# Kernel optimization log

Hardware: AMD Instinct MI355X
Metric: run time of the kernel (lower is better)

Reference implementation:

```python
import jax, jax.numpy as jnp
import numpy as np

K = 9          # kernel_size (number of KNN neighbours), dilation=1
SCALAR = 20.0  # scalar in _build_explain
EPS = 1e-10


def setup_inputs() -> dict:
    key = jax.random.key(0)
    ks = jax.random.split(key, 9)
    B, C, H, W = 16, 192, 28, 28
    Cout, r = 384, 16
    f = lambda k, s, sc: jax.random.normal(k, s, jnp.float32) * sc
    return {
        "x": f(ks[0], (B, C, H, W), 1.0),
        "w_edge": f(ks[1], (Cout, 2 * C), 0.05),  # 1x1 conv on concat[x_i, x_j-x_i]
        "b_edge": f(ks[2], (Cout,), 0.05),
        "w1": f(ks[3], (C // r, C), 0.1),          # CBAM channel MLP (shared)
        "b1": f(ks[4], (C // r,), 0.1),
        "w2": f(ks[5], (C, C // r), 0.1),
        "b2": f(ks[6], (C,), 0.1),
        "w_sp": f(ks[7], (1, 2, 7, 7), 0.1),       # CBAM spatial 7x7 conv
        "b_sp": f(ks[8], (1,), 0.1),
    }


def _cbam(x, w1, b1, w2, b2, w_sp, b_sp):
    # Standard CBAM: channel gate (avg+max pooled -> shared MLP -> sigmoid)
    # then spatial gate (channel mean/max -> 7x7 conv -> sigmoid).
    mlp = lambda v: jax.nn.relu(v @ w1.T + b1) @ w2.T + b2
    ch = jax.nn.sigmoid(mlp(x.mean((2, 3))) + mlp(x.max((2, 3))))
    x = x * ch[:, :, None, None]
    sp_in = jnp.stack([x.mean(1), x.max(1)], axis=1)  # (B,2,H,W)
    sp = jax.lax.conv_general_dilated(sp_in, w_sp, (1, 1), [(3, 3), (3, 3)])
    return x * jax.nn.sigmoid(sp + b_sp[None, :, None, None])


def _build_explain(att_x):
    B, C, H, W = att_x.shape
    a = jax.nn.softmax(att_x.reshape(B, C, H * W), axis=2)
    a = a / (a.max(axis=2, keepdims=True) + EPS)
    return (2.0 * a - 1.0) / (2.0 * SCALAR) + 1.0  # (B,C,N)


def _knn_idx(xf):
    # DenseDilatedKnnGraph: L2-normalize over channels, pairwise sq-dist, topk.
    xn = xf / jnp.maximum(jnp.linalg.norm(xf, axis=1, keepdims=True), 1e-12)
    xt = jnp.swapaxes(xn, 1, 2)                      # (B,N,C)
    sq = jnp.sum(xt * xt, axis=-1)                   # (B,N)
    dist = sq[:, :, None] - 2.0 * jnp.einsum("bnc,bmc->bnm", xt, xt) + sq[:, None, :]
    _, idx = jax.lax.top_k(-dist, K)                 # nn_idx = edge_index[0], (B,N,K)
    return idx


def reference(x, w_edge, b_edge, w1, b1, w2, b2, w_sp, b_sp):
    B, C, H, W = x.shape
    N = H * W
    xf = x.reshape(B, C, N)
    idx = _knn_idx(xf)                               # dynamic KNN graph (B,N,K)
    att = _build_explain(_cbam(x, w1, b1, w2, b2, w_sp, b_sp))
    xf = xf * att
    # EdgeConv2d: x_i = center (edge_index[1] is arange -> broadcast),
    # x_j gathered by neighbour indices.
    x_i = xf[:, :, :, None]                           # (B,C,N,1)
    x_e = jnp.broadcast_to(x_i, (B, C, N, K))
    i_e = jnp.broadcast_to(idx[:, None, :, :], (B, C, N, K))
    x_j = jnp.take_along_axis(x_e, i_e, axis=2)       # (B,C,N,K)
    feat = jnp.concatenate([x_e, x_j - x_i], axis=1)  # (B,2C,N,K)
    out = jnp.einsum("oc,bcnk->bonk", w_edge, feat) + b_edge[None, :, None, None]
    out = jax.nn.relu(out)                            # BasicConv: 1x1 conv + relu
    out = out.max(axis=-1)                            # max over neighbours (B,O,N)
    return out.reshape(B, -1, H, W)
```

## Files before the change

kernel.cpp:

```cpp
#include <hip/hip_runtime.h>
#include <math.h>

#define HW 784
#define Cc 192
#define Bb 16
#define CO 384
#define KK 9
#define OG 8

typedef __attribute__((ext_vector_type(8))) short bf16x8;
typedef __attribute__((ext_vector_type(4))) float f32x4;

__device__ __forceinline__ unsigned f2ord(float f){
  unsigned u = __float_as_uint(f);
  return (u & 0x80000000u) ? ~u : (u | 0x80000000u);
}

__device__ __forceinline__ unsigned short b16rne(float v){
  unsigned u = __float_as_uint(v);
  unsigned r = u + 0x7FFFu + ((u >> 16) & 1u);
  return (unsigned short)(r >> 16);
}

__global__ void k_chstats(const float* __restrict__ x, float* __restrict__ chm, float* __restrict__ chx){
  int wid = threadIdx.x >> 6, lane = threadIdx.x & 63;
  int r = blockIdx.x * 4 + wid;
  const float* row = x + (size_t)r * HW;
  float s = 0.f, m = -3.4e38f;
  for (int n = lane; n < HW; n += 64){ float v = row[n]; s += v; m = fmaxf(m, v); }
  for (int off = 32; off; off >>= 1){ s += __shfl_xor(s, off); m = fmaxf(m, __shfl_xor(m, off)); }
  if (lane == 0){ chm[r] = s / (float)HW; chx[r] = m; }
}

__global__ void k_mlp(const float* __restrict__ chm, const float* __restrict__ chx,
                      const float* __restrict__ w1, const float* __restrict__ b1,
                      const float* __restrict__ w2, const float* __restrict__ b2,
                      float* __restrict__ chv){
  int b = blockIdx.x, t = threadIdx.x;
  __shared__ float vm[Cc], vx[Cc], hp[2][12];
  if (t < Cc){ vm[t] = chm[b*Cc + t]; vx[t] = chx[b*Cc + t]; }
  __syncthreads();
  if (t < 24){
    int h = t % 12;
    const float* src = (t < 12) ? vm : vx;
    float a = b1[h];
    for (int c = 0; c < Cc; ++c) a += src[c] * w1[h*Cc + c];
    hp[t/12][h] = fmaxf(a, 0.f);
  }
  __syncthreads();
  if (t < Cc){
    float a = 2.f * b2[t];
    for (int h = 0; h < 12; ++h) a += (hp[0][h] + hp[1][h]) * w2[t*12 + h];
    chv[b*Cc + t] = 1.f / (1.f + expf(-a));
  }
}

__global__ void k_spin(const float* __restrict__ x, const float* __restrict__ chv,
                       float* __restrict__ amean, float* __restrict__ amax){
  int b = blockIdx.x >> 2;
  int n = ((blockIdx.x & 3) << 8) + threadIdx.x;
  if (n >= HW) return;
  const float* xb = x + (size_t)b*Cc*HW + n;
  const float* cb = chv + b*Cc;
  float s = 0.f, m = -3.4e38f;
  for (int c = 0; c < Cc; ++c){ float v = xb[(size_t)c*HW] * cb[c]; s += v; m = fmaxf(m, v); }
  amean[b*HW + n] = s / (float)Cc;
  amax[b*HW + n]  = m;
}

__global__ void k_conv(const float* __restrict__ amean, const float* __restrict__ amax,
                       const float* __restrict__ wsp, const float* __restrict__ bsp,
                       float* __restrict__ satt){
  int b = blockIdx.x >> 2;
  int n = ((blockIdx.x & 3) << 8) + threadIdx.x;
  if (n >= HW) return;
  int yy = n / 28, xx = n % 28;
  float a = 0.f;
  for (int ky = 0; ky < 7; ++ky){
    int iy = yy + ky - 3; if (iy < 0 || iy >= 28) continue;
    for (int kx = 0; kx < 7; ++kx){
      int ix = xx + kx - 3; if (ix < 0 || ix >= 28) continue;
      int ii = b*HW + iy*28 + ix;
      a += amean[ii]*wsp[ky*7 + kx] + amax[ii]*wsp[49 + ky*7 + kx];
    }
  }
  satt[b*HW + n] = 1.f / (1.f + expf(-(a + bsp[0])));
}

__global__ __launch_bounds__(256) void k_att(const float* __restrict__ x, const float* __restrict__ chv,
                                             const float* __restrict__ satt, float* __restrict__ xatt){
  int bc = blockIdx.x;
  int b = bc / Cc;
  int t = threadIdx.x, wid = t >> 6, lane = t & 63;
  const float* xr = x + (size_t)bc * HW;
  const float* sr = satt + b * HW;
  float ch = chv[bc];
  float xv[4], vv[4];
  float lmax = -3.4e38f;
  #pragma unroll
  for (int j = 0; j < 4; ++j){
    int n = t + 256*j;
    if (n < HW){
      xv[j] = xr[n];
      float t1 = xv[j] * ch;
      vv[j] = t1 * sr[n];
      lmax = fmaxf(lmax, vv[j]);
    }
  }
  __shared__ float red[8];
  for (int off = 32; off; off >>= 1) lmax = fmaxf(lmax, __shfl_xor(lmax, off));
  if (!lane) red[wid] = lmax;
  __syncthreads();
  float vmax = fmaxf(fmaxf(red[0], red[1]), fmaxf(red[2], red[3]));
  float ls = 0.f;
  #pragma unroll
  for (int j = 0; j < 4; ++j){
    int n = t + 256*j;
    if (n < HW){ vv[j] = expf(vv[j] - vmax); ls += vv[j]; }
  }
  for (int off = 32; off; off >>= 1) ls += __shfl_xor(ls, off);
  if (!lane) red[4 + wid] = ls;
  __syncthreads();
  float S = red[4] + red[5] + red[6] + red[7];
  float inv = 1.f / (1.f + 1e-10f * S);
  #pragma unroll
  for (int j = 0; j < 4; ++j){
    int n = t + 256*j;
    if (n < HW){
      float a = vv[j] * inv;
      xatt[(size_t)bc*HW + n] = xv[j] * ((2.f*a - 1.f)*0.025f + 1.f);
    }
  }
}

__global__ void k_norm(const float* __restrict__ x, float* __restrict__ nrm){
  int b = blockIdx.x >> 2;
  int n = ((blockIdx.x & 3) << 8) + threadIdx.x;
  if (n >= HW) return;
  const float* xb = x + (size_t)b*Cc*HW + n;
  float s = 0.f;
  for (int c = 0; c < Cc; ++c){ float v = xb[(size_t)c*HW]; s += v*v; }
  nrm[b*HW + n] = fmaxf(sqrtf(s), 1e-12f);
}

__global__ __launch_bounds__(256) void k_cvt(const float* __restrict__ x, const float* __restrict__ nrm,
                                             unsigned short* __restrict__ Xth, unsigned short* __restrict__ Xtl){
  int b = blockIdx.z, c0 = blockIdx.y*64, n0 = blockIdx.x*64;
  __shared__ float T[64][65];
  int t = threadIdx.x;
  int nl = (t & 15) * 4, cl = t >> 4;
  const float* xb = x + (size_t)b*Cc*HW;
  #pragma unroll
  for (int r = 0; r < 4; ++r){
    int c_loc = cl + r*16;
    int n = n0 + nl;
    float4 v = (n < HW) ? *(const float4*)(xb + (size_t)(c0 + c_loc)*HW + n) : make_float4(0,0,0,0);
    *(float4*)&T[c_loc][nl] = v;
  }
  __syncthreads();
  int nr = t >> 2, q = t & 3;
  int n_g = n0 + nr;
  if (n_g >= HW) return;
  float nv = nrm ? nrm[b*HW + n_g] : 1.f;
  unsigned int hw_[8], lw_[8];
  #pragma unroll
  for (int j = 0; j < 8; ++j){
    float v0 = T[q*16 + 2*j][nr] / nv;
    float v1 = T[q*16 + 2*j + 1][nr] / nv;
    unsigned short h0 = b16rne(v0), h1 = b16rne(v1);
    float l0 = v0 - __uint_as_float((unsigned)h0 << 16);
    float l1 = v1 - __uint_as_float((unsigned)h1 << 16);
    hw_[j] = (unsigned)h0 | ((unsigned)h1 << 16);
    lw_[j] = (unsigned)b16rne(l0) | ((unsigned)b16rne(l1) << 16);
  }
  size_t base = ((size_t)b*HW + n_g)*Cc + c0 + q*16;
  *(uint4*)(Xth + base)     = make_uint4(hw_[0], hw_[1], hw_[2], hw_[3]);
  *(uint4*)(Xth + base + 8) = make_uint4(hw_[4], hw_[5], hw_[6], hw_[7]);
  *(uint4*)(Xtl + base)     = make_uint4(lw_[0], lw_[1], lw_[2], lw_[3]);
  *(uint4*)(Xtl + base + 8) = make_uint4(lw_[4], lw_[5], lw_[6], lw_[7]);
}

__global__ __launch_bounds__(256) void k_gram(const unsigned short* __restrict__ Xth,
                                              const unsigned short* __restrict__ Xtl,
                                              float* __restrict__ D){
  int b = blockIdx.z;
  int n0 = blockIdx.y*128, m0 = blockIdx.x*128;
  __shared__ unsigned short Als[8192];
  __shared__ unsigned short Bls[8192];
  int t = threadIdx.x, w = t >> 6, l = t & 63;
  int wr = w >> 1, wc = w & 1;
  f32x4 acc[4][4] = {};
  int nn = t >> 1, half = t & 1;
  size_t bb = (size_t)b*HW*Cc;
  int ra = n0 + nn; if (ra > HW-1) ra = HW-1;
  int rb = m0 + nn; if (rb > HW-1) rb = HW-1;

  for (int cc = 0; cc < 9; ++cc){
    int seg = cc/3, kc0 = (cc%3)*64;
    const unsigned short* As_ = (seg < 2 ? Xth : Xtl) + bb;
    const unsigned short* Bs_ = (seg == 1 ? Xtl : Xth) + bb;
    const uint4* ga = (const uint4*)(As_ + (size_t)ra*Cc + kc0 + half*32);
    const uint4* gb = (const uint4*)(Bs_ + (size_t)rb*Cc + kc0 + half*32);
    uint4 va0 = ga[0], va1 = ga[1], va2 = ga[2], va3 = ga[3];
    uint4 vb0 = gb[0], vb1 = gb[1], vb2 = gb[2], vb3 = gb[3];
    __syncthreads();
    int base = nn*128 + half*64;
    int sw = (nn & 7) << 4;
    *(uint4*)((char*)Als + ((base      ) ^ sw)) = va0;
    *(uint4*)((char*)Als + ((base + 16 ) ^ sw)) = va1;
    *(uint4*)((char*)Als + ((base + 32 ) ^ sw)) = va2;
    *(uint4*)((char*)Als + ((base + 48 ) ^ sw)) = va3;
    *(uint4*)((char*)Bls + ((base      ) ^ sw)) = vb0;
    *(uint4*)((char*)Bls + ((base + 16 ) ^ sw)) = vb1;
    *(uint4*)((char*)Bls + ((base + 32 ) ^ sw)) = vb2;
    *(uint4*)((char*)Bls + ((base + 48 ) ^ sw)) = vb3;
    __syncthreads();
    #pragma unroll
    for (int ks = 0; ks < 2; ++ks){
      bf16x8 af[4], bfr[4];
      int kb = ks*64 + (l >> 4)*16;
      #pragma unroll
      for (int mt = 0; mt < 4; ++mt){
        int rl = wr*64 + mt*16 + (l & 15);
        int off = (rl*128 + kb) ^ ((rl & 7) << 4);
        af[mt] = *(const bf16x8*)((const char*)Als + off);
      }
      #pragma unroll
      for (int nt = 0; nt < 4; ++nt){
        int cl2 = wc*64 + nt*16 + (l & 15);
        int off = (cl2*128 + kb) ^ ((cl2 & 7) << 4);
        bfr[nt] = *(const bf16x8*)((const char*)Bls + off);
      }
      #pragma unroll
      for (int mt = 0; mt < 4; ++mt)
        #pragma unroll
        for (int nt = 0; nt < 4; ++nt)
          acc[mt][nt] = __builtin_amdgcn_mfma_f32_16x16x32_bf16(af[mt], bfr[nt], acc[mt][nt], 0, 0, 0);
    }
  }
  #pragma unroll
  for (int mt = 0; mt < 4; ++mt){
    #pragma unroll
    for (int nt = 0; nt < 4; ++nt){
      int col = m0 + wc*64 + nt*16 + (l & 15);
      if (col >= HW) continue;
      int row0 = n0 + wr*64 + mt*16 + ((l >> 4) << 2);
      #pragma unroll
      for (int r = 0; r < 4; ++r){
        int row = row0 + r;
        if (row < HW) D[((size_t)b*HW + row)*HW + col] = -acc[mt][nt][r];
      }
    }
  }
}

__global__ __launch_bounds__(256) void k_select(const float* __restrict__ D, int* __restrict__ idxo){
  int wid = threadIdx.x >> 6, lane = threadIdx.x & 63;
  int row = blockIdx.x * 4 + wid;
  const float* Dr = D + (size_t)row * HW;
  float dvv[13]; int mvv[13];
  #pragma unroll
  for (int i = 0; i < 13; ++i){
    int m = lane + 64*i;
    dvv[i] = (m < HW) ? Dr[m] : 3.4e38f;
    mvv[i] = m;
  }
  for (int k = 0; k < KK; ++k){
    float bd = dvv[0]; int bi = 0;
    #pragma unroll
    for (int i = 1; i < 13; ++i) if (dvv[i] < bd){ bd = dvv[i]; bi = i; }
    unsigned long long key = ((unsigned long long)f2ord(bd) << 32) | (unsigned)mvv[bi];
    for (int off = 32; off; off >>= 1){
      unsigned long long o = __shfl_xor(key, off);
      if (o < key) key = o;
    }
    int wm = (int)(unsigned)(key & 0xffffffffu);
    if (lane == 0) idxo[(size_t)k*(Bb*HW) + row] = wm;
    if (mvv[bi] == wm) dvv[bi] = 3.4e38f;
  }
}

__global__ void k_wp(const float* __restrict__ we, unsigned short* __restrict__ Wph,
                     unsigned short* __restrict__ Wpl){
  int i = blockIdx.x*256 + threadIdx.x;
  if (i >= 768*Cc) return;
  int o = i / Cc, c = i % Cc;
  float v = (o < CO) ? (we[(size_t)o*384 + c] - we[(size_t)o*384 + Cc + c])
                     : we[(size_t)(o - CO)*384 + Cc + c];
  unsigned short h = b16rne(v);
  float lo = v - __uint_as_float((unsigned)h << 16);
  Wph[i] = h;
  Wpl[i] = b16rne(lo);
}

__global__ __launch_bounds__(256) void k_gemm2(const unsigned short* __restrict__ Wph,
                                               const unsigned short* __restrict__ Wpl,
                                               const unsigned short* __restrict__ XAh,
                                               const unsigned short* __restrict__ XAl,
                                               float* __restrict__ PQ){
  int b = blockIdx.z;
  int o0 = blockIdx.y*128, n0 = blockIdx.x*128;
  __shared__ unsigned short Als[8192];
  __shared__ unsigned short Bls[8192];
  int t = threadIdx.x, w = t >> 6, l = t & 63;
  int wr = w >> 1, wc = w & 1;
  f32x4 acc[4][4] = {};
  int nn = t >> 1, half = t & 1;
  size_t bx = (size_t)b*HW*Cc;
  int ra = o0 + nn;
  int rb = n0 + nn; if (rb > HW-1) rb = HW-1;

  for (int cc = 0; cc < 9; ++cc){
    int seg = cc/3, kc0 = (cc%3)*64;
    const unsigned short* As_ = (seg < 2 ? Wph : Wpl);
    const unsigned short* Bs_ = (seg == 1 ? XAl : XAh) + bx;
    const uint4* ga = (const uint4*)(As_ + (size_t)ra*Cc + kc0 + half*32);
    const uint4* gb = (const uint4*)(Bs_ + (size_t)rb*Cc + kc0 + half*32);
    uint4 va0 = ga[0], va1 = ga[1], va2 = ga[2], va3 = ga[3];
    uint4 vb0 = gb[0], vb1 = gb[1], vb2 = gb[2], vb3 = gb[3];
    __syncthreads();
    int base = nn*128 + half*64;
    int sw = (nn & 7) << 4;
    *(uint4*)((char*)Als + ((base      ) ^ sw)) = va0;
    *(uint4*)((char*)Als + ((base + 16 ) ^ sw)) = va1;
    *(uint4*)((char*)Als + ((base + 32 ) ^ sw)) = va2;
    *(uint4*)((char*)Als + ((base + 48 ) ^ sw)) = va3;
    *(uint4*)((char*)Bls + ((base      ) ^ sw)) = vb0;
    *(uint4*)((char*)Bls + ((base + 16 ) ^ sw)) = vb1;
    *(uint4*)((char*)Bls + ((base + 32 ) ^ sw)) = vb2;
    *(uint4*)((char*)Bls + ((base + 48 ) ^ sw)) = vb3;
    __syncthreads();
    #pragma unroll
    for (int ks = 0; ks < 2; ++ks){
      bf16x8 af[4], bfr[4];
      int kb = ks*64 + (l >> 4)*16;
      #pragma unroll
      for (int mt = 0; mt < 4; ++mt){
        int rl = wr*64 + mt*16 + (l & 15);
        int off = (rl*128 + kb) ^ ((rl & 7) << 4);
        af[mt] = *(const bf16x8*)((const char*)Als + off);
      }
      #pragma unroll
      for (int nt = 0; nt < 4; ++nt){
        int cl2 = wc*64 + nt*16 + (l & 15);
        int off = (cl2*128 + kb) ^ ((cl2 & 7) << 4);
        bfr[nt] = *(const bf16x8*)((const char*)Bls + off);
      }
      #pragma unroll
      for (int mt = 0; mt < 4; ++mt)
        #pragma unroll
        for (int nt = 0; nt < 4; ++nt)
          acc[mt][nt] = __builtin_amdgcn_mfma_f32_16x16x32_bf16(af[mt], bfr[nt], acc[mt][nt], 0, 0, 0);
    }
  }
  #pragma unroll
  for (int mt = 0; mt < 4; ++mt){
    #pragma unroll
    for (int nt = 0; nt < 4; ++nt){
      int col = n0 + wc*64 + nt*16 + (l & 15);
      if (col >= HW) continue;
      int row0 = o0 + wr*64 + mt*16 + ((l >> 4) << 2);
      #pragma unroll
      for (int r = 0; r < 4; ++r){
        PQ[((size_t)b*768 + row0 + r)*HW + col] = acc[mt][nt][r];
      }
    }
  }
}

__global__ __launch_bounds__(256) void k_edge(const float* __restrict__ PQ, const int* __restrict__ idx,
                                              const float* __restrict__ be, float* __restrict__ out){
  int bid = blockIdx.x;
  int b = bid / (CO/OG), og = bid % (CO/OG);
  int o0 = og * OG;
  __shared__ float Qls[OG][HW + 4];
  const float* Qbase = PQ + ((size_t)b*768 + CO + o0)*HW;
  int t = threadIdx.x;
  #pragma unroll
  for (int oo = 0; oo < OG; ++oo){
    if (t < 196) *(float4*)&Qls[oo][t*4] = *(const float4*)(Qbase + (size_t)oo*HW + t*4);
  }
  __syncthreads();
  const float* Pbase = PQ + ((size_t)b*768 + o0)*HW;
  float bev[OG];
  #pragma unroll
  for (int oo = 0; oo < OG; ++oo) bev[oo] = be[o0 + oo];
  for (int n = t; n < HW; n += 256){
    int ip[KK];
    #pragma unroll
    for (int k = 0; k < KK; ++k) ip[k] = idx[(size_t)k*(Bb*HW) + b*HW + n];
    float qm[OG];
    #pragma unroll
    for (int oo = 0; oo < OG; ++oo) qm[oo] = -3.4e38f;
    #pragma unroll
    for (int k = 0; k < KK; ++k){
      int j = ip[k];
      #pragma unroll
      for (int oo = 0; oo < OG; ++oo) qm[oo] = fmaxf(qm[oo], Qls[oo][j]);
    }
    #pragma unroll
    for (int oo = 0; oo < OG; ++oo){
      out[((size_t)b*CO + o0 + oo)*HW + n] = fmaxf(Pbase[(size_t)oo*HW + n] + bev[oo] + qm[oo], 0.f);
    }
  }
}

extern "C" void kernel_launch(void* const* d_in, const int* in_sizes, int n_in,
                              void* d_out, int out_size, void* d_ws, size_t ws_size,
                              hipStream_t stream){
  const float* x   = (const float*)d_in[0];
  const float* we  = (const float*)d_in[1];
  const float* be  = (const float*)d_in[2];
  const float* w1  = (const float*)d_in[3];
  const float* b1  = (const float*)d_in[4];
  const float* w2  = (const float*)d_in[5];
  const float* b2  = (const float*)d_in[6];
  const float* wsp = (const float*)d_in[7];
  const float* bsp = (const float*)d_in[8];
  float* out = (float*)d_out;

  float* ws    = (float*)d_ws;
  float* chm   = ws;
  float* chx   = chm + 3072;
  float* chv   = chx + 3072;
  float* amean = chv + 3072;
  float* amax  = amean + 12544;
  float* satt  = amax + 12544;
  float* nrm   = satt + 12544;
  unsigned short* Wph = (unsigned short*)(nrm + 12544);
  unsigned short* Wpl = Wph + 147456;
  float* xatt  = (float*)(Wpl + 147456);
  unsigned short* Xth = (unsigned short*)(xatt + 2408448);
  unsigned short* Xtl = Xth + 2408448;
  int*   idx   = (int*)(Xtl + 2408448);
  float* D     = (float*)(idx + 112896);
  float* PQ    = D;

  k_chstats<<<768, 256, 0, stream>>>(x, chm, chx);
  k_mlp<<<16, 192, 0, stream>>>(chm, chx, w1, b1, w2, b2, chv);
  k_spin<<<64, 256, 0, stream>>>(x, chv, amean, amax);
  k_conv<<<64, 256, 0, stream>>>(amean, amax, wsp, bsp, satt);
  k_att<<<3072, 256, 0, stream>>>(x, chv, satt, xatt);
  k_norm<<<64, 256, 0, stream>>>(x, nrm);
  k_cvt<<<dim3(13, 3, 16), 256, 0, stream>>>(x, nrm, Xth, Xtl);
  k_gram<<<dim3(7, 7, 16), 256, 0, stream>>>(Xth, Xtl, D);
  k_select<<<3136, 256, 0, stream>>>(D, idx);
  k_wp<<<576, 256, 0, stream>>>(we, Wph, Wpl);
  k_cvt<<<dim3(13, 3, 16), 256, 0, stream>>>(xatt, nullptr, Xth, Xtl);
  k_gemm2<<<dim3(7, 6, 16), 256, 0, stream>>>(Wph, Wpl, Xth, Xtl, PQ);
  k_edge<<<Bb*(CO/OG), 256, 0, stream>>>(PQ, idx, be, out);
}
```

Measured before the change: 172.7 us.

## Fuse norm into spin, split attention into stats plus fused dual bf16 conversion

Computes the per-pixel L2 norm inside k_spin so k_norm disappears. The attention kernel becomes a stats-only pass that stores the per-row max and inverse scale. A single k_cvt2 then reads x once and writes both the normalized and the attention-scaled hi/lo bf16 transposes, so the fp32 xatt buffer, its round trip and one conversion launch are gone. In exchange, exp is recomputed in the conversion kernel and there are now two passes over x instead of the fused att pass.

```diff
diff --git a/kernel.cpp b/kernel.cpp
--- a/kernel.cpp
+++ b/kernel.cpp
@@ -56,16 +56,22 @@
 }
 
 __global__ void k_spin(const float* __restrict__ x, const float* __restrict__ chv,
-                       float* __restrict__ amean, float* __restrict__ amax){
+                       float* __restrict__ amean, float* __restrict__ amax,
+                       float* __restrict__ nrm){
   int b = blockIdx.x >> 2;
   int n = ((blockIdx.x & 3) << 8) + threadIdx.x;
   if (n >= HW) return;
   const float* xb = x + (size_t)b*Cc*HW + n;
   const float* cb = chv + b*Cc;
-  float s = 0.f, m = -3.4e38f;
-  for (int c = 0; c < Cc; ++c){ float v = xb[(size_t)c*HW] * cb[c]; s += v; m = fmaxf(m, v); }
+  float s = 0.f, m = -3.4e38f, sq = 0.f;
+  for (int c = 0; c < Cc; ++c){
+    float xv = xb[(size_t)c*HW];
+    float v = xv * cb[c];
+    s += v; m = fmaxf(m, v); sq += xv*xv;
+  }
   amean[b*HW + n] = s / (float)Cc;
   amax[b*HW + n]  = m;
+  nrm[b*HW + n]   = fmaxf(sqrtf(sq), 1e-12f);
 }
 
 __global__ void k_conv(const float* __restrict__ amean, const float* __restrict__ amax,
@@ -87,66 +93,42 @@
   satt[b*HW + n] = 1.f / (1.f + expf(-(a + bsp[0])));
 }
 
-__global__ __launch_bounds__(256) void k_att(const float* __restrict__ x, const float* __restrict__ chv,
-                                             const float* __restrict__ satt, float* __restrict__ xatt){
-  int bc = blockIdx.x;
-  int b = bc / Cc;
-  int t = threadIdx.x, wid = t >> 6, lane = t & 63;
-  const float* xr = x + (size_t)bc * HW;
+__global__ void k_attstats(const float* __restrict__ x, const float* __restrict__ chv,
+                           const float* __restrict__ satt,
+                           float* __restrict__ vmaxA, float* __restrict__ invA){
+  int wid = threadIdx.x >> 6, lane = threadIdx.x & 63;
+  int r = blockIdx.x * 4 + wid;
+  int b = r / Cc;
+  const float* row = x + (size_t)r * HW;
   const float* sr = satt + b * HW;
-  float ch = chv[bc];
-  float xv[4], vv[4];
-  float lmax = -3.4e38f;
-  #pragma unroll
-  for (int j = 0; j < 4; ++j){
-    int n = t + 256*j;
-    if (n < HW){
-      xv[j] = xr[n];
-      float t1 = xv[j] * ch;
-      vv[j] = t1 * sr[n];
-      lmax = fmaxf(lmax, vv[j]);
-    }
-  }
-  __shared__ float red[8];
-  for (int off = 32; off; off >>= 1) lmax = fmaxf(lmax, __shfl_xor(lmax, off));
-  if (!lane) red[wid] = lmax;
-  __syncthreads();
-  float vmax = fmaxf(fmaxf(red[0], red[1]), fmaxf(red[2], red[3]));
-  float ls = 0.f;
-  #pragma unroll
-  for (int j = 0; j < 4; ++j){
-    int n = t + 256*j;
-    if (n < HW){ vv[j] = expf(vv[j] - vmax); ls += vv[j]; }
-  }
-  for (int off = 32; off; off >>= 1) ls += __shfl_xor(ls, off);
-  if (!lane) red[4 + wid] = ls;
-  __syncthreads();
-  float S = red[4] + red[5] + red[6] + red[7];
-  float inv = 1.f / (1.f + 1e-10f * S);
-  #pragma unroll
-  for (int j = 0; j < 4; ++j){
-    int n = t + 256*j;
-    if (n < HW){
-      float a = vv[j] * inv;
-      xatt[(size_t)bc*HW + n] = xv[j] * ((2.f*a - 1.f)*0.025f + 1.f);
-    }
-  }
-}
-
-__global__ void k_norm(const float* __restrict__ x, float* __restrict__ nrm){
-  int b = blockIdx.x >> 2;
-  int n = ((blockIdx.x & 3) << 8) + threadIdx.x;
-  if (n >= HW) return;
-  const float* xb = x + (size_t)b*Cc*HW + n;
+  float ch = chv[r];
+  float vv[13];
+  float m = -3.4e38f;
+  #pragma unroll
+  for (int i = 0; i < 13; ++i){
+    int n = lane + 64*i;
+    vv[i] = (n < HW) ? (row[n] * ch) * sr[n] : -3.4e38f;
+    m = fmaxf(m, vv[i]);
+  }
+  for (int off = 32; off; off >>= 1) m = fmaxf(m, __shfl_xor(m, off));
   float s = 0.f;
-  for (int c = 0; c < Cc; ++c){ float v = xb[(size_t)c*HW]; s += v*v; }
-  nrm[b*HW + n] = fmaxf(sqrtf(s), 1e-12f);
-}
-
-__global__ __launch_bounds__(256) void k_cvt(const float* __restrict__ x, const float* __restrict__ nrm,
-                                             unsigned short* __restrict__ Xth, unsigned short* __restrict__ Xtl){
+  #pragma unroll
+  for (int i = 0; i < 13; ++i){
+    int n = lane + 64*i;
+    if (n < HW) s += expf(vv[i] - m);
+  }
+  for (int off = 32; off; off >>= 1) s += __shfl_xor(s, off);
+  if (lane == 0){ vmaxA[r] = m; invA[r] = 1.f / (1.f + 1e-10f * s); }
+}
+
+__global__ __launch_bounds__(256) void k_cvt2(const float* __restrict__ x, const float* __restrict__ nrm,
+                                              const float* __restrict__ chv, const float* __restrict__ satt,
+                                              const float* __restrict__ vmaxA, const float* __restrict__ invA,
+                                              unsigned short* __restrict__ Xnh, unsigned short* __restrict__ Xnl,
+                                              unsigned short* __restrict__ XAh, unsigned short* __restrict__ XAl){
   int b = blockIdx.z, c0 = blockIdx.y*64, n0 = blockIdx.x*64;
   __shared__ float T[64][65];
+  __shared__ float chs[64], vms[64], ivs[64];
   int t = threadIdx.x;
   int nl = (t & 15) * 4, cl = t >> 4;
   const float* xb = x + (size_t)b*Cc*HW;
@@ -157,27 +139,51 @@
     float4 v = (n < HW) ? *(const float4*)(xb + (size_t)(c0 + c_loc)*HW + n) : make_float4(0,0,0,0);
     *(float4*)&T[c_loc][nl] = v;
   }
+  if (t < 64){
+    chs[t] = chv[b*Cc + c0 + t];
+    vms[t] = vmaxA[b*Cc + c0 + t];
+    ivs[t] = invA[b*Cc + c0 + t];
+  }
   __syncthreads();
   int nr = t >> 2, q = t & 3;
   int n_g = n0 + nr;
   if (n_g >= HW) return;
-  float nv = nrm ? nrm[b*HW + n_g] : 1.f;
-  unsigned int hw_[8], lw_[8];
+  float nv = nrm[b*HW + n_g];
+  float sr = satt[b*HW + n_g];
+  unsigned int nh[8], nlw[8], ah[8], al[8];
   #pragma unroll
   for (int j = 0; j < 8; ++j){
-    float v0 = T[q*16 + 2*j][nr] / nv;
-    float v1 = T[q*16 + 2*j + 1][nr] / nv;
-    unsigned short h0 = b16rne(v0), h1 = b16rne(v1);
-    float l0 = v0 - __uint_as_float((unsigned)h0 << 16);
-    float l1 = v1 - __uint_as_float((unsigned)h1 << 16);
-    hw_[j] = (unsigned)h0 | ((unsigned)h1 << 16);
-    lw_[j] = (unsigned)b16rne(l0) | ((unsigned)b16rne(l1) << 16);
+    unsigned int parts[2][2];
+    #pragma unroll
+    for (int e = 0; e < 2; ++e){
+      int cc_ = q*16 + 2*j + e;
+      float v = T[cc_][nr];
+      float xnv = v / nv;
+      unsigned short h0 = b16rne(xnv);
+      float l0 = xnv - __uint_as_float((unsigned)h0 << 16);
+      parts[0][e] = (unsigned)h0 | ((unsigned)b16rne(l0) << 16);
+      float vvv = (v * chs[cc_]) * sr;
+      float ex = expf(vvv - vms[cc_]);
+      float a = ex * ivs[cc_];
+      float xav = v * ((2.f*a - 1.f)*0.025f + 1.f);
+      unsigned short h1 = b16rne(xav);
+      float l1 = xav - __uint_as_float((unsigned)h1 << 16);
+      parts[1][e] = (unsigned)h1 | ((unsigned)b16rne(l1) << 16);
+    }
+    nh[j]  = (parts[0][0] & 0xFFFFu) | (parts[0][1] << 16);
+    nlw[j] = (parts[0][0] >> 16)     | (parts[0][1] & 0xFFFF0000u);
+    ah[j]  = (parts[1][0] & 0xFFFFu) | (parts[1][1] << 16);
+    al[j]  = (parts[1][0] >> 16)     | (parts[1][1] & 0xFFFF0000u);
   }
   size_t base = ((size_t)b*HW + n_g)*Cc + c0 + q*16;
-  *(uint4*)(Xth + base)     = make_uint4(hw_[0], hw_[1], hw_[2], hw_[3]);
-  *(uint4*)(Xth + base + 8) = make_uint4(hw_[4], hw_[5], hw_[6], hw_[7]);
-  *(uint4*)(Xtl + base)     = make_uint4(lw_[0], lw_[1], lw_[2], lw_[3]);
-  *(uint4*)(Xtl + base + 8) = make_uint4(lw_[4], lw_[5], lw_[6], lw_[7]);
+  *(uint4*)(Xnh + base)     = make_uint4(nh[0], nh[1], nh[2], nh[3]);
+  *(uint4*)(Xnh + base + 8) = make_uint4(nh[4], nh[5], nh[6], nh[7]);
+  *(uint4*)(Xnl + base)     = make_uint4(nlw[0], nlw[1], nlw[2], nlw[3]);
+  *(uint4*)(Xnl + base + 8) = make_uint4(nlw[4], nlw[5], nlw[6], nlw[7]);
+  *(uint4*)(XAh + base)     = make_uint4(ah[0], ah[1], ah[2], ah[3]);
+  *(uint4*)(XAh + base + 8) = make_uint4(ah[4], ah[5], ah[6], ah[7]);
+  *(uint4*)(XAl + base)     = make_uint4(al[0], al[1], al[2], al[3]);
+  *(uint4*)(XAl + base + 8) = make_uint4(al[4], al[5], al[6], al[7]);
 }
 
 __global__ __launch_bounds__(256) void k_gram(const unsigned short* __restrict__ Xth,
@@ -423,30 +429,31 @@
   float* chm   = ws;
   float* chx   = chm + 3072;
   float* chv   = chx + 3072;
-  float* amean = chv + 3072;
+  float* vmaxA = chv + 3072;
+  float* invA  = vmaxA + 3072;
+  float* amean = invA + 3072;
   float* amax  = amean + 12544;
   float* satt  = amax + 12544;
   float* nrm   = satt + 12544;
   unsigned short* Wph = (unsigned short*)(nrm + 12544);
   unsigned short* Wpl = Wph + 147456;
-  float* xatt  = (float*)(Wpl + 147456);
-  unsigned short* Xth = (unsigned short*)(xatt + 2408448);
-  unsigned short* Xtl = Xth + 2408448;
-  int*   idx   = (int*)(Xtl + 2408448);
+  unsigned short* Xnh = Wpl + 147456;
+  unsigned short* Xnl = Xnh + 2408448;
+  unsigned short* XAh = Xnl + 2408448;
+  unsigned short* XAl = XAh + 2408448;
+  int*   idx   = (int*)(XAl + 2408448);
   float* D     = (float*)(idx + 112896);
   float* PQ    = D;
 
   k_chstats<<<768, 256, 0, stream>>>(x, chm, chx);
   k_mlp<<<16, 192, 0, stream>>>(chm, chx, w1, b1, w2, b2, chv);
-  k_spin<<<64, 256, 0, stream>>>(x, chv, amean, amax);
+  k_spin<<<64, 256, 0, stream>>>(x, chv, amean, amax, nrm);
   k_conv<<<64, 256, 0, stream>>>(amean, amax, wsp, bsp, satt);
-  k_att<<<3072, 256, 0, stream>>>(x, chv, satt, xatt);
-  k_norm<<<64, 256, 0, stream>>>(x, nrm);
-  k_cvt<<<dim3(13, 3, 16), 256, 0, stream>>>(x, nrm, Xth, Xtl);
-  k_gram<<<dim3(7, 7, 16), 256, 0, stream>>>(Xth, Xtl, D);
+  k_attstats<<<768, 256, 0, stream>>>(x, chv, satt, vmaxA, invA);
+  k_cvt2<<<dim3(13, 3, 16), 256, 0, stream>>>(x, nrm, chv, satt, vmaxA, invA, Xnh, Xnl, XAh, XAl);
+  k_gram<<<dim3(7, 7, 16), 256, 0, stream>>>(Xnh, Xnl, D);
   k_select<<<3136, 256, 0, stream>>>(D, idx);
   k_wp<<<576, 256, 0, stream>>>(we, Wph, Wpl);
-  k_cvt<<<dim3(13, 3, 16), 256, 0, stream>>>(xatt, nullptr, Xth, Xtl);
-  k_gemm2<<<dim3(7, 6, 16), 256, 0, stream>>>(Wph, Wpl, Xth, Xtl, PQ);
+  k_gemm2<<<dim3(7, 6, 16), 256, 0, stream>>>(Wph, Wpl, XAh, XAl, PQ);
   k_edge<<<Bb*(CO/OG), 256, 0, stream>>>(PQ, idx, be, out);
 }
```

Measured after the change: 159.3 us. 7.8% less time.
